# Kernel optimization log

Measured on AMD Instinct MI355X. Metric: run time of the kernel, lower is better.

## Reference

```python
import jax, jax.numpy as jnp
import numpy as np


def _conv3x3(x, w, stride=1):
    # x: [N, C_in, H, W], w: [C_out, C_in, 3, 3] (ternary {-1,0,1}), padding=1, no bias
    return jax.lax.conv_general_dilated(
        x, w,
        window_strides=(stride, stride),
        padding=((1, 1), (1, 1)),
        dimension_numbers=("NCHW", "OIHW", "NCHW"),
    )


def _bn(x, gamma, beta, mean, var, eps=1e-5):
    # inference-mode BatchNorm2d over channel dim
    inv = gamma * jax.lax.rsqrt(var + eps)
    return x * inv[None, :, None, None] + (beta - mean * inv)[None, :, None, None]


def setup_inputs() -> dict:
    key = jax.random.key(0)
    ks = jax.random.split(key, 8)
    N, C, H, W = 64, 256, 32, 32
    x = jax.random.normal(ks[0], (N, C, H, W), dtype=jnp.float32)
    # Ternary conv weights in {-1, 0, +1} (scale_and_shift=False => raw ternary values)
    w1 = jax.random.randint(ks[1], (C, C, 3, 3), -1, 2).astype(jnp.float32)
    w2 = jax.random.randint(ks[2], (C, C, 3, 3), -1, 2).astype(jnp.float32)
    # BatchNorm affine params and running stats
    g1 = jax.random.normal(ks[3], (C,), dtype=jnp.float32) * 0.1 + 1.0
    b1 = jax.random.normal(ks[4], (C,), dtype=jnp.float32) * 0.1
    g2 = jax.random.normal(ks[5], (C,), dtype=jnp.float32) * 0.1 + 1.0
    b2 = jax.random.normal(ks[6], (C,), dtype=jnp.float32) * 0.1
    rm1 = jnp.zeros((C,), dtype=jnp.float32)
    rv1 = jnp.ones((C,), dtype=jnp.float32)
    rm2 = jnp.zeros((C,), dtype=jnp.float32)
    rv2 = jnp.ones((C,), dtype=jnp.float32)
    return {"x": x, "w1": w1, "g1": g1, "b1": b1, "rm1": rm1, "rv1": rv1,
            "w2": w2, "g2": g2, "b2": b2, "rm2": rm2, "rv2": rv2}


def reference(x, w1, g1, b1, rm1, rv1, w2, g2, b2, rm2, rv2):
    # BasicBlock forward: stride=1, downsample=None -> identity skip
    h = _conv3x3(x, w1, stride=1)
    h = _bn(h, g1, b1, rm1, rv1)
    h = jax.nn.relu(h)
    h = _conv3x3(h, w2, stride=1)
    h = _bn(h, g2, b2, rm2, rv2)
    return jax.nn.relu(x + h)
```

## Files before the change

### kernel.cpp

```cpp
#include <hip/hip_runtime.h>

typedef unsigned short u16;
typedef unsigned int u32;
typedef __attribute__((ext_vector_type(8))) short bf16x8;
typedef __attribute__((ext_vector_type(4))) float f32x4;

__device__ __forceinline__ u16 f2bf(float f) {
    u32 u = __float_as_uint(f);
    u += 0x7fffu + ((u >> 16) & 1u);
    return (u16)(u >> 16);
}

__device__ __forceinline__ void llds16(void* l, const void* g) {
    __builtin_amdgcn_global_load_lds(
        (const __attribute__((address_space(1))) u32*)g,
        (__attribute__((address_space(3))) u32*)l, 16, 0, 0);
}

__global__ void prep(const float* __restrict__ x, u16* __restrict__ xt,
                     const float* __restrict__ w1, const float* __restrict__ w2,
                     u16* __restrict__ W1t, u16* __restrict__ W2t,
                     const float* __restrict__ g1, const float* __restrict__ b1,
                     const float* __restrict__ rm1, const float* __restrict__ rv1,
                     const float* __restrict__ g2, const float* __restrict__ b2,
                     const float* __restrict__ rm2, const float* __restrict__ rv2,
                     float* __restrict__ sc, u32* __restrict__ zp) {
    int t = threadIdx.x;
    int b = blockIdx.x;
    if (b < 16384) {
        __shared__ float xl[32 * 33];
        int n = b >> 8, rem = b & 255;
        int h = rem >> 3, c0 = (rem & 7) << 5;
        int cl = t >> 5, w = t & 31;
#pragma unroll
        for (int i = 0; i < 4; ++i) {
            int c = c0 + i * 8 + cl;
            xl[(i * 8 + cl) * 33 + w] = x[(n * 256 + c) * 1024 + h * 32 + w];
        }
        __syncthreads();
        int wo = t >> 3, k = t & 7;
        ushort4 o;
        o.x = f2bf(xl[(k * 4 + 0) * 33 + wo]);
        o.y = f2bf(xl[(k * 4 + 1) * 33 + wo]);
        o.z = f2bf(xl[(k * 4 + 2) * 33 + wo]);
        o.w = f2bf(xl[(k * 4 + 3) * 33 + wo]);
        *(ushort4*)&xt[((n * 32 + h) * 32 + wo) * 256 + c0 + k * 4] = o;
    } else {
        int bb = b - 16384;
        int idx = (bb & 255) * 256 + t;
        const float* src = (bb >> 8) ? w2 : w1;
        u16* dst = (bb >> 8) ? W2t : W1t;
        const float* s = src + idx * 9;
        int co = idx >> 8, ci = idx & 255;
#pragma unroll
        for (int p = 0; p < 9; ++p)
            dst[p * 65536 + co * 256 + ci] = f2bf(s[p]);
        if (bb == 0) {
            float s1 = g1[t] * rsqrtf(rv1[t] + 1e-5f);
            sc[t]       = s1;
            sc[256 + t] = b1[t] - rm1[t] * s1;
            float s2 = g2[t] * rsqrtf(rv2[t] + 1e-5f);
            sc[512 + t] = s2;
            sc[768 + t] = b2[t] - rm2[t] * s2;
            zp[t] = 0u;
            zp[t + 256] = 0u;
        }
    }
}

__global__ __launch_bounds__(256, 2) void conv_mfma(
    const u16* __restrict__ Xt,
    const u16* __restrict__ Wt,
    const float* __restrict__ sv,
    const float* __restrict__ tv,
    const float* __restrict__ skip,
    u16* __restrict__ ybf,
    float* __restrict__ yf,
    const u16* __restrict__ zp, int stage)
{
    __shared__ alignas(16) u16 ldsA[9 * 4 * 64 * 8];
    __shared__ alignas(16) u16 ldsB[22 * 64 * 8];

    int t = threadIdx.x;
    int wv = t >> 6, lane = t & 63;
    int q = lane >> 4, n16 = lane & 15;

    int bid = blockIdx.x;
    int co_t = (bid >> 3) & 3;
    int sp   = ((bid >> 5) << 3) | (bid & 7);
    int h_t  = sp & 3, nb = sp >> 2;
    int co0 = co_t << 6, h0 = h_t << 3;

    const u16* aSrc[9];
#pragma unroll
    for (int i = 0; i < 9; ++i) {
        int g = wv * 9 + i;
        int p = g >> 2, mt = g & 3;
        aSrc[i] = Wt + (p << 16) + ((co0 + (mt << 4) + n16) << 8) + (q << 3);
    }
    const u16* bSrc[6];
#pragma unroll
    for (int j = 0; j < 6; ++j) {
        int g2 = wv * 6 + j;
        if (g2 < 22) {
            int s = g2 * 64 + lane;
            int hi = s / 136, rem = s - hi * 136;
            int wp = rem >> 2, qq = rem & 3;
            int hin = h0 - 1 + hi;
            bool v = (wp >= 1) && (wp <= 32) && (hin >= 0) && (hin < 32);
            bSrc[j] = v ? (Xt + (((nb << 5) + hin) * 32 + (wp - 1)) * 256 + (qq << 3))
                        : (zp + lane * 8);
        } else {
            bSrc[j] = zp + lane * 8;
        }
    }

    f32x4 acc[4][4] = {};

#pragma unroll
    for (int i = 0; i < 9; ++i)
        llds16(&ldsA[(wv * 9 + i) << 9], aSrc[i]);
#pragma unroll
    for (int j = 0; j < 6; ++j) {
        int g2 = wv * 6 + j;
        if (g2 < 22) llds16(&ldsB[g2 << 9], bSrc[j]);
    }

    for (int kt = 0; kt < 8; ++kt) {
        asm volatile("s_waitcnt vmcnt(0)" ::: "memory");
        __builtin_amdgcn_s_barrier();

#pragma unroll
        for (int kw = 0; kw < 2; ++kw) {
            bf16x8 bFr[4][2];
#pragma unroll
            for (int r = 0; r < 4; ++r)
#pragma unroll
                for (int half = 0; half < 2; ++half) {
                    int hi = (wv << 1) + r;
                    int wp = (half << 4) + n16 + kw;
                    bFr[r][half] = *(const bf16x8*)
                        &ldsB[(hi * 136 + (wp << 2) + q) << 3];
                }
            __builtin_amdgcn_s_setprio(1);
#pragma unroll
            for (int kh = 0; kh < 3; ++kh) {
                int p = kh * 3 + kw;
                bf16x8 aF[4];
#pragma unroll
                for (int mt = 0; mt < 4; ++mt)
                    aF[mt] = *(const bf16x8*)&ldsA[((p << 8) + (mt << 6) + lane) << 3];
#pragma unroll
                for (int mt = 0; mt < 4; ++mt)
#pragma unroll
                    for (int nt = 0; nt < 4; ++nt)
                        acc[mt][nt] = __builtin_amdgcn_mfma_f32_16x16x32_bf16(
                            aF[mt], bFr[(nt >> 1) + kh][nt & 1], acc[mt][nt], 0, 0, 0);
            }
            __builtin_amdgcn_s_setprio(0);
        }

        bf16x8 bF2[4][2];
        bf16x8 aF2[3][4];
#pragma unroll
        for (int r = 0; r < 4; ++r)
#pragma unroll
            for (int half = 0; half < 2; ++half) {
                int hi = (wv << 1) + r;
                int wp = (half << 4) + n16 + 2;
                bF2[r][half] = *(const bf16x8*)
                    &ldsB[(hi * 136 + (wp << 2) + q) << 3];
            }
#pragma unroll
        for (int kh = 0; kh < 3; ++kh) {
            int p = kh * 3 + 2;
#pragma unroll
            for (int mt = 0; mt < 4; ++mt)
                aF2[kh][mt] = *(const bf16x8*)&ldsA[((p << 8) + (mt << 6) + lane) << 3];
        }
        asm volatile("s_waitcnt lgkmcnt(0)" ::: "memory");
        __builtin_amdgcn_sched_barrier(0);
        __builtin_amdgcn_s_barrier();

        if (kt < 7) {
            int kc = (kt + 1) << 5;
#pragma unroll
            for (int i = 0; i < 9; ++i)
                llds16(&ldsA[(wv * 9 + i) << 9], aSrc[i] + kc);
#pragma unroll
            for (int j = 0; j < 6; ++j) {
                int g2 = wv * 6 + j;
                if (g2 < 22) llds16(&ldsB[g2 << 9], bSrc[j] + kc);
            }
        }
        __builtin_amdgcn_sched_barrier(0);

        __builtin_amdgcn_s_setprio(1);
#pragma unroll
        for (int kh = 0; kh < 3; ++kh)
#pragma unroll
            for (int mt = 0; mt < 4; ++mt)
#pragma unroll
                for (int nt = 0; nt < 4; ++nt)
                    acc[mt][nt] = __builtin_amdgcn_mfma_f32_16x16x32_bf16(
                        aF2[kh][mt], bF2[(nt >> 1) + kh][nt & 1], acc[mt][nt], 0, 0, 0);
        __builtin_amdgcn_s_setprio(0);
    }

    if (stage == 1) {
#pragma unroll
        for (int mt = 0; mt < 4; ++mt) {
            int cb = co0 + (mt << 4) + (q << 2);
            f32x4 ss = *(const f32x4*)&sv[cb];
            f32x4 tt = *(const f32x4*)&tv[cb];
#pragma unroll
            for (int nt = 0; nt < 4; ++nt) {
                int h = h0 + (wv << 1) + (nt >> 1), w = ((nt & 1) << 4) + n16;
                ushort4 o;
                o.x = f2bf(fmaxf(acc[mt][nt][0] * ss[0] + tt[0], 0.f));
                o.y = f2bf(fmaxf(acc[mt][nt][1] * ss[1] + tt[1], 0.f));
                o.z = f2bf(fmaxf(acc[mt][nt][2] * ss[2] + tt[2], 0.f));
                o.w = f2bf(fmaxf(acc[mt][nt][3] * ss[3] + tt[3], 0.f));
                *(ushort4*)&ybf[(((nb << 5) + h) * 32 + w) * 256 + cb] = o;
            }
        }
    } else {
#pragma unroll
        for (int mt = 0; mt < 4; ++mt) {
            int cb = co0 + (mt << 4) + (q << 2);
            f32x4 ss = *(const f32x4*)&sv[cb];
            f32x4 tt = *(const f32x4*)&tv[cb];
#pragma unroll
            for (int nt = 0; nt < 4; ++nt) {
                int h = h0 + (wv << 1) + (nt >> 1), w = ((nt & 1) << 4) + n16;
#pragma unroll
                for (int j = 0; j < 4; ++j) {
                    int idx = (((nb << 8) + cb + j) << 10) + (h << 5) + w;
                    yf[idx] = fmaxf(acc[mt][nt][j] * ss[j] + tt[j] + skip[idx], 0.f);
                }
            }
        }
    }
}

extern "C" void kernel_launch(void* const* d_in, const int* in_sizes, int n_in,
                              void* d_out, int out_size, void* d_ws, size_t ws_size,
                              hipStream_t stream) {
    const float* x   = (const float*)d_in[0];
    const float* w1  = (const float*)d_in[1];
    const float* g1  = (const float*)d_in[2];
    const float* b1  = (const float*)d_in[3];
    const float* rm1 = (const float*)d_in[4];
    const float* rv1 = (const float*)d_in[5];
    const float* w2  = (const float*)d_in[6];
    const float* g2  = (const float*)d_in[7];
    const float* b2  = (const float*)d_in[8];
    const float* rm2 = (const float*)d_in[9];
    const float* rv2 = (const float*)d_in[10];

    char* ws = (char*)d_ws;
    u16*  XT  = (u16*)(ws);
    u16*  H1  = (u16*)(ws + 33554432);
    u16*  W1t = (u16*)(ws + 67108864);
    u16*  W2t = (u16*)(ws + 68288512);
    float* sc = (float*)(ws + 69468160);
    u32*  zpg = (u32*)(ws + 69472256);
    if (ws_size < 69474304) return;

    prep<<<16896, 256, 0, stream>>>(x, XT, w1, w2, W1t, W2t,
                                    g1, b1, rm1, rv1, g2, b2, rm2, rv2,
                                    sc, zpg);

    conv_mfma<<<1024, 256, 0, stream>>>(XT, W1t, sc, sc + 256, nullptr,
                                        H1, nullptr, (const u16*)zpg, 1);
    conv_mfma<<<1024, 256, 0, stream>>>(H1, W2t, sc + 512, sc + 768, x,
                                        nullptr, (float*)d_out, (const u16*)zpg, 2);
}
```

Baseline: 267.5 us.

## Keep two weight taps in registers to shrink LDS and raise occupancy

```diff
diff --git a/kernel.cpp b/kernel.cpp
--- a/kernel.cpp
+++ b/kernel.cpp
@@ -68,7 +68,7 @@
     }
 }
 
-__global__ __launch_bounds__(256, 2) void conv_mfma(
+__global__ __launch_bounds__(256, 3) void conv_mfma(
     const u16* __restrict__ Xt,
     const u16* __restrict__ Wt,
     const float* __restrict__ sv,
@@ -78,7 +78,7 @@
     float* __restrict__ yf,
     const u16* __restrict__ zp, int stage)
 {
-    __shared__ alignas(16) u16 ldsA[9 * 4 * 64 * 8];
+    __shared__ alignas(16) u16 ldsA[7 * 4 * 64 * 8];
     __shared__ alignas(16) u16 ldsB[22 * 64 * 8];
 
     int t = threadIdx.x;
@@ -91,12 +91,19 @@
     int h_t  = sp & 3, nb = sp >> 2;
     int co0 = co_t << 6, h0 = h_t << 3;
 
-    const u16* aSrc[9];
-#pragma unroll
-    for (int i = 0; i < 9; ++i) {
-        int g = wv * 9 + i;
+    const u16* aSrc[7];
+#pragma unroll
+    for (int i = 0; i < 7; ++i) {
+        int g = wv * 7 + i;
         int p = g >> 2, mt = g & 3;
         aSrc[i] = Wt + (p << 16) + ((co0 + (mt << 4) + n16) << 8) + (q << 3);
+    }
+    const u16* a7Src[4];
+    const u16* a8Src[4];
+#pragma unroll
+    for (int mt = 0; mt < 4; ++mt) {
+        a7Src[mt] = Wt + (7 << 16) + ((co0 + (mt << 4) + n16) << 8) + (q << 3);
+        a8Src[mt] = Wt + (8 << 16) + ((co0 + (mt << 4) + n16) << 8) + (q << 3);
     }
     const u16* bSrc[6];
 #pragma unroll
@@ -116,22 +123,28 @@
     }
 
     f32x4 acc[4][4] = {};
-
-#pragma unroll
-    for (int i = 0; i < 9; ++i)
-        llds16(&ldsA[(wv * 9 + i) << 9], aSrc[i]);
+    bf16x8 Ap7[4], Ap8[4];
+
+#pragma unroll
+    for (int i = 0; i < 7; ++i)
+        llds16(&ldsA[(wv * 7 + i) << 9], aSrc[i]);
 #pragma unroll
     for (int j = 0; j < 6; ++j) {
         int g2 = wv * 6 + j;
         if (g2 < 22) llds16(&ldsB[g2 << 9], bSrc[j]);
     }
+#pragma unroll
+    for (int mt = 0; mt < 4; ++mt) {
+        Ap7[mt] = *(const bf16x8*)(a7Src[mt]);
+        Ap8[mt] = *(const bf16x8*)(a8Src[mt]);
+    }
 
     for (int kt = 0; kt < 8; ++kt) {
         asm volatile("s_waitcnt vmcnt(0)" ::: "memory");
         __builtin_amdgcn_s_barrier();
 
 #pragma unroll
-        for (int kw = 0; kw < 2; ++kw) {
+        for (int kw = 1; kw <= 2; ++kw) {
             bf16x8 bFr[4][2];
 #pragma unroll
             for (int r = 0; r < 4; ++r)
@@ -145,11 +158,13 @@
             __builtin_amdgcn_s_setprio(1);
 #pragma unroll
             for (int kh = 0; kh < 3; ++kh) {
-                int p = kh * 3 + kw;
+                const int p = kh * 3 + kw;
                 bf16x8 aF[4];
 #pragma unroll
                 for (int mt = 0; mt < 4; ++mt)
-                    aF[mt] = *(const bf16x8*)&ldsA[((p << 8) + (mt << 6) + lane) << 3];
+                    aF[mt] = (p <= 6)
+                        ? *(const bf16x8*)&ldsA[((p << 8) + (mt << 6) + lane) << 3]
+                        : ((p == 7) ? Ap7[mt] : Ap8[mt]);
 #pragma unroll
                 for (int mt = 0; mt < 4; ++mt)
 #pragma unroll
@@ -167,13 +182,13 @@
 #pragma unroll
             for (int half = 0; half < 2; ++half) {
                 int hi = (wv << 1) + r;
-                int wp = (half << 4) + n16 + 2;
+                int wp = (half << 4) + n16;
                 bF2[r][half] = *(const bf16x8*)
                     &ldsB[(hi * 136 + (wp << 2) + q) << 3];
             }
 #pragma unroll
         for (int kh = 0; kh < 3; ++kh) {
-            int p = kh * 3 + 2;
+            const int p = kh * 3;
 #pragma unroll
             for (int mt = 0; mt < 4; ++mt)
                 aF2[kh][mt] = *(const bf16x8*)&ldsA[((p << 8) + (mt << 6) + lane) << 3];
@@ -185,12 +200,17 @@
         if (kt < 7) {
             int kc = (kt + 1) << 5;
 #pragma unroll
-            for (int i = 0; i < 9; ++i)
-                llds16(&ldsA[(wv * 9 + i) << 9], aSrc[i] + kc);
+            for (int i = 0; i < 7; ++i)
+                llds16(&ldsA[(wv * 7 + i) << 9], aSrc[i] + kc);
 #pragma unroll
             for (int j = 0; j < 6; ++j) {
                 int g2 = wv * 6 + j;
                 if (g2 < 22) llds16(&ldsB[g2 << 9], bSrc[j] + kc);
+            }
+#pragma unroll
+            for (int mt = 0; mt < 4; ++mt) {
+                Ap7[mt] = *(const bf16x8*)(a7Src[mt] + kc);
+                Ap8[mt] = *(const bf16x8*)(a8Src[mt] + kc);
             }
         }
         __builtin_amdgcn_sched_barrier(0);
```

After: 543.0 us. 2.03x slower.
